# Kernel tuning notes

Hardware: AMD Instinct MI355X
Metric: run time of the kernel (lower is better)

## Reference

```python
import jax, jax.numpy as jnp
import numpy as np

N, E = 50000, 600000
IN, H, O, HEADS = 14, 128, 64, 4
EPS = 1e-5


def layer_norm(x, g, b):
    m = jnp.mean(x, axis=-1, keepdims=True)
    v = jnp.mean((x - m) ** 2, axis=-1, keepdims=True)
    return (x - m) * jax.lax.rsqrt(v + EPS) * g + b


def sage_conv(x, src, dst, W_l, b_l, W_r):
    # mean aggregation of source messages at destination, then lin_l(agg)+lin_r(x)
    s = jax.ops.segment_sum(x[src], dst, num_segments=N)            # [N,H]
    cnt = jax.ops.segment_sum(jnp.ones((src.shape[0],), x.dtype), dst, num_segments=N)
    agg = s / jnp.maximum(cnt, 1.0)[:, None]
    return agg @ W_l + b_l + x @ W_r


def gat_conv(x, src, dst, W_g, att_src, att_dst, b_g):
    # PyG GATConv with add_self_loops=True, heads=4, concat=False -> head mean
    loop = jnp.arange(N, dtype=src.dtype)
    s2 = jnp.concatenate([src, loop])
    d2 = jnp.concatenate([dst, loop])
    h = (x @ W_g).reshape(N, HEADS, O)                               # [N,4,64]
    a_s = jnp.sum(h * att_src, axis=-1)                              # [N,4]
    a_d = jnp.sum(h * att_dst, axis=-1)
    e = jax.nn.leaky_relu(a_s[s2] + a_d[d2], negative_slope=0.2)     # [E+N,4]
    m = jax.ops.segment_max(e, d2, num_segments=N)
    ex = jnp.exp(e - m[d2])
    den = jax.ops.segment_sum(ex, d2, num_segments=N)
    alpha = ex / den[d2]                                             # edge softmax
    out = jax.ops.segment_sum(h[s2] * alpha[..., None], d2, num_segments=N)
    return jnp.mean(out, axis=1) + b_g                               # [N,64]


def setup_inputs() -> dict:
    key = jax.random.key(0)
    ks = jax.random.split(key, 18)
    sc = 0.05
    return {
        'x': jax.random.normal(ks[0], (N, IN), jnp.float32),
        'edge_index': jax.random.randint(ks[1], (2, E), 0, N, dtype=jnp.int64),
        'W_in': jax.random.normal(ks[2], (IN, H), jnp.float32) * sc,
        'b_in': jnp.zeros((H,), jnp.float32),
        'W1_l': jax.random.normal(ks[3], (H, H), jnp.float32) * sc,
        'b1': jnp.zeros((H,), jnp.float32),
        'W1_r': jax.random.normal(ks[4], (H, H), jnp.float32) * sc,
        'g1': jnp.ones((H,), jnp.float32),
        'be1': jnp.zeros((H,), jnp.float32),
        'W2_l': jax.random.normal(ks[5], (H, H), jnp.float32) * sc,
        'b2': jnp.zeros((H,), jnp.float32),
        'W2_r': jax.random.normal(ks[6], (H, H), jnp.float32) * sc,
        'g2': jnp.ones((H,), jnp.float32),
        'be2': jnp.zeros((H,), jnp.float32),
        'W_g': jax.random.normal(ks[7], (H, HEADS * O), jnp.float32) * sc,
        'att_src': jax.random.normal(ks[8], (HEADS, O), jnp.float32) * sc,
        'att_dst': jax.random.normal(ks[9], (HEADS, O), jnp.float32) * sc,
        'b_g': jnp.zeros((O,), jnp.float32),
        'g3': jnp.ones((O,), jnp.float32),
        'be3': jnp.zeros((O,), jnp.float32),
    }


def reference(x, edge_index, W_in, b_in, W1_l, b1, W1_r, g1, be1,
              W2_l, b2, W2_r, g2, be2, W_g, att_src, att_dst, b_g, g3, be3):
    src, dst = edge_index[0], edge_index[1]
    h = jax.nn.relu(x @ W_in + b_in)                 # input_proj + relu (dropout: eval)
    # layer 0: SAGE + LN + relu + residual
    h_res = h
    h = jax.nn.relu(layer_norm(sage_conv(h, src, dst, W1_l, b1, W1_r), g1, be1)) + h_res
    # layer 1: SAGE + LN + relu + residual
    h_res = h
    h = jax.nn.relu(layer_norm(sage_conv(h, src, dst, W2_l, b2, W2_r), g2, be2)) + h_res
    # layer 2 (last): GAT + LN, no relu/residual (shape changes H->O anyway)
    h = layer_norm(gat_conv(h, src, dst, W_g, att_src, att_dst, b_g), g3, be3)
    return h
```

## Files before the change

### kernel.cpp

```cpp
#include <hip/hip_runtime.h>
#include <math.h>

#define EPSV 1e-5f

typedef __attribute__((ext_vector_type(8))) short short8;
typedef __attribute__((ext_vector_type(4))) float f32x4;

__device__ __forceinline__ unsigned short f2b(float f) {
  union { float f; unsigned int u; } c; c.f = f;
  unsigned int u = c.u + 0x7fffu + ((c.u >> 16) & 1u);
  return (unsigned short)(u >> 16);
}
__device__ __forceinline__ float b2f(unsigned short h) {
  union { unsigned int u; float f; } c; c.u = ((unsigned int)h) << 16;
  return c.f;
}
__device__ __forceinline__ float ub(unsigned int w, int j) {
  return (float)((w >> (8 * j)) & 0xffu);
}

__global__ void k_prep3(const float* __restrict__ Wl, const float* __restrict__ Wr,
                        const float* __restrict__ Wg, unsigned short* __restrict__ WlT,
                        unsigned short* __restrict__ WrT, unsigned short* __restrict__ WgT) {
  int id = blockIdx.x * 256 + threadIdx.x;
  if (id < 16384) {
    int n = id >> 7, k = id & 127;
    WlT[id] = f2b(Wl[k * 128 + n]);
  } else if (id < 32768) {
    int j = id - 16384; int n = j >> 7, k = j & 127;
    WrT[j] = f2b(Wr[k * 128 + n]);
  } else {
    int j = id - 32768; int n = j >> 7, k = j & 127;
    WgT[j] = f2b(Wg[k * 256 + n]);
  }
}
__global__ void k_prep2(const float* __restrict__ Wl, const float* __restrict__ Wr,
                        unsigned short* __restrict__ WlT, unsigned short* __restrict__ WrT) {
  int id = blockIdx.x * 256 + threadIdx.x;
  if (id < 16384) {
    int n = id >> 7, k = id & 127;
    WlT[id] = f2b(Wl[k * 128 + n]);
  } else {
    int j = id - 16384; int n = j >> 7, k = j & 127;
    WrT[j] = f2b(Wr[k * 128 + n]);
  }
}

__global__ void k_proj(const float* __restrict__ x, const float* __restrict__ W,
                       const float* __restrict__ b, unsigned short* __restrict__ h16,
                       unsigned char* __restrict__ h8, float2* __restrict__ hmeta, int nN) {
  int t = blockIdx.x * 256 + threadIdx.x;
  int n = t >> 6;
  if (n >= nN) return;
  int lane = t & 63;
  const float* xr = x + (size_t)n * 14;
  float acc0 = b[lane], acc1 = b[lane + 64];
#pragma unroll
  for (int k = 0; k < 14; ++k) {
    float xv = xr[k];
    acc0 = fmaf(xv, W[k * 128 + lane], acc0);
    acc1 = fmaf(xv, W[k * 128 + lane + 64], acc1);
  }
  float o0 = fmaxf(acc0, 0.f), o1 = fmaxf(acc1, 0.f);
  h16[(size_t)n * 128 + lane] = f2b(o0);
  h16[(size_t)n * 128 + lane + 64] = f2b(o1);
  float rmin = fminf(o0, o1), rmax = fmaxf(o0, o1);
#pragma unroll
  for (int m = 1; m <= 32; m <<= 1) {
    rmin = fminf(rmin, __shfl_xor(rmin, m));
    rmax = fmaxf(rmax, __shfl_xor(rmax, m));
  }
  float scale = (rmax - rmin) * (1.f / 255.f);
  float invq = (rmax > rmin) ? 255.f / (rmax - rmin) : 0.f;
  h8[(size_t)n * 128 + lane] = (unsigned char)(int)rintf((o0 - rmin) * invq);
  h8[(size_t)n * 128 + lane + 64] = (unsigned char)(int)rintf((o1 - rmin) * invq);
  if (lane == 0) hmeta[n] = make_float2(scale, rmin);
}

__global__ void k_count_int(const int* __restrict__ dst, int* __restrict__ cnt, int E_) {
  int e = blockIdx.x * 256 + threadIdx.x;
  if (e < E_) atomicAdd(&cnt[dst[e]], 1);
}

__global__ void k_scan1(const int* __restrict__ cnt, int* __restrict__ incl,
                        int* __restrict__ bsum, int nN) {
  __shared__ int sh[256];
  int tid = threadIdx.x;
  int i = blockIdx.x * 256 + tid;
  int v = (i < nN) ? cnt[i] : 0;
  sh[tid] = v;
  __syncthreads();
#pragma unroll
  for (int off = 1; off < 256; off <<= 1) {
    int t = (tid >= off) ? sh[tid - off] : 0;
    __syncthreads();
    sh[tid] += t;
    __syncthreads();
  }
  if (i < nN) incl[i] = sh[tid];
  if (tid == 255) bsum[blockIdx.x] = sh[255];
}

__global__ void k_scan2(int* __restrict__ bsum, int nb) {
  __shared__ int sh[256];
  int tid = threadIdx.x;
  int v = (tid < nb) ? bsum[tid] : 0;
  sh[tid] = v;
  __syncthreads();
#pragma unroll
  for (int off = 1; off < 256; off <<= 1) {
    int t = (tid >= off) ? sh[tid - off] : 0;
    __syncthreads();
    sh[tid] += t;
    __syncthreads();
  }
  if (tid < nb) bsum[tid] = sh[tid] - v;
}

__global__ void k_scan3(const int* __restrict__ incl, const int* __restrict__ bsum,
                        const int* __restrict__ cnt, int* __restrict__ rowptr, int nN) {
  int i = blockIdx.x * 256 + threadIdx.x;
  if (i < nN) rowptr[i] = incl[i] - cnt[i] + bsum[blockIdx.x];
}

__global__ void k_fill(const int* __restrict__ src, const int* __restrict__ dst,
                       const int* __restrict__ rowptr, int* __restrict__ cursor,
                       int* __restrict__ eSrc, int E_) {
  int e = blockIdx.x * 256 + threadIdx.x;
  if (e >= E_) return;
  int d = dst[e];
  int pos = rowptr[d] + atomicAdd(&cursor[d], 1);
  eSrc[pos] = src[e];
}

__global__ void k_sage_gather8(const unsigned char* __restrict__ h8,
                               const float2* __restrict__ hmeta,
                               const int* __restrict__ rowptr, const int* __restrict__ cnt,
                               const int* __restrict__ eSrc,
                               unsigned short* __restrict__ agg16, int nN) {
  int t = blockIdx.x * 256 + threadIdx.x;
  int n = t >> 4;
  if (n >= nN) return;
  int sub = t & 15;
  int fo = sub * 8;
  int beg = rowptr[n], c = cnt[n];
  float a0[8], a1[8], a2[8], a3[8];
#pragma unroll
  for (int j = 0; j < 8; ++j) { a0[j] = 0.f; a1[j] = 0.f; a2[j] = 0.f; a3[j] = 0.f; }
  float m0 = 0.f, m1 = 0.f, m2 = 0.f, m3 = 0.f;
  int i = 0;
  for (; i + 4 <= c; i += 4) {
    int s0 = eSrc[beg + i], s1 = eSrc[beg + i + 1];
    int s2 = eSrc[beg + i + 2], s3 = eSrc[beg + i + 3];
    float2 t0 = hmeta[s0], t1 = hmeta[s1], t2 = hmeta[s2], t3 = hmeta[s3];
    uint2 p0 = *(const uint2*)(h8 + (size_t)s0 * 128 + fo);
    uint2 p1 = *(const uint2*)(h8 + (size_t)s1 * 128 + fo);
    uint2 p2 = *(const uint2*)(h8 + (size_t)s2 * 128 + fo);
    uint2 p3 = *(const uint2*)(h8 + (size_t)s3 * 128 + fo);
#pragma unroll
    for (int j = 0; j < 4; ++j) {
      a0[j] = fmaf(t0.x, ub(p0.x, j), a0[j]);
      a1[j] = fmaf(t1.x, ub(p1.x, j), a1[j]);
      a2[j] = fmaf(t2.x, ub(p2.x, j), a2[j]);
      a3[j] = fmaf(t3.x, ub(p3.x, j), a3[j]);
      a0[j + 4] = fmaf(t0.x, ub(p0.y, j), a0[j + 4]);
      a1[j + 4] = fmaf(t1.x, ub(p1.y, j), a1[j + 4]);
      a2[j + 4] = fmaf(t2.x, ub(p2.y, j), a2[j + 4]);
      a3[j + 4] = fmaf(t3.x, ub(p3.y, j), a3[j + 4]);
    }
    m0 += t0.y; m1 += t1.y; m2 += t2.y; m3 += t3.y;
  }
  for (; i < c; ++i) {
    int s = eSrc[beg + i];
    float2 tm = hmeta[s];
    uint2 p = *(const uint2*)(h8 + (size_t)s * 128 + fo);
#pragma unroll
    for (int j = 0; j < 4; ++j) {
      a0[j] = fmaf(tm.x, ub(p.x, j), a0[j]);
      a0[j + 4] = fmaf(tm.x, ub(p.y, j), a0[j + 4]);
    }
    m0 += tm.y;
  }
  float mm = (m0 + m1) + (m2 + m3);
  float inv = 1.f / fmaxf((float)c, 1.f);
  short8 r;
#pragma unroll
  for (int j = 0; j < 8; ++j)
    r[j] = (short)f2b((((a0[j] + a1[j]) + (a2[j] + a3[j])) + mm) * inv);
  *(short8*)(agg16 + (size_t)n * 128 + fo) = r;
}

__global__ __launch_bounds__(256)
void k_sage_mfma(const unsigned short* __restrict__ agg16,
                 const unsigned short* __restrict__ hin16,
                 const unsigned short* __restrict__ WlT,
                 const unsigned short* __restrict__ WrT,
                 const float* __restrict__ bias, const float* __restrict__ gam,
                 const float* __restrict__ bet,
                 unsigned short* __restrict__ hout16,
                 unsigned char* __restrict__ hout8, float2* __restrict__ hmeta_o,
                 int quant, int nN) {
  __shared__ unsigned short lA[64][136];
  __shared__ unsigned short lB[128][136];
  int tid = threadIdx.x;
  int wave = tid >> 6, lane = tid & 63;
  int cl = lane & 15, g = lane >> 4;
  int rowBase = blockIdx.x * 64;
  f32x4 acc[8];
#pragma unroll
  for (int ct = 0; ct < 8; ++ct) acc[ct] = (f32x4){0.f, 0.f, 0.f, 0.f};

  int ar = tid >> 2, ap = (tid & 3) * 32;
  int br = tid >> 1, bp = (tid & 1) * 64;

  for (int half = 0; half < 2; ++half) {
    const unsigned short* At = half ? hin16 : agg16;
    const unsigned short* Bt = half ? WrT : WlT;
    if (half) __syncthreads();
    {
      int grow = rowBase + ar;
      if (grow < nN) {
        const unsigned short* sp = At + (size_t)grow * 128 + ap;
#pragma unroll
        for (int u = 0; u < 4; ++u)
          *(short8*)&lA[ar][ap + u * 8] = *(const short8*)(sp + u * 8);
      } else {
        short8 z = {0, 0, 0, 0, 0, 0, 0, 0};
#pragma unroll
        for (int u = 0; u < 4; ++u) *(short8*)&lA[ar][ap + u * 8] = z;
      }
      const unsigned short* bsp = Bt + (size_t)br * 128 + bp;
#pragma unroll
      for (int u = 0; u < 8; ++u)
        *(short8*)&lB[br][bp + u * 8] = *(const short8*)(bsp + u * 8);
    }
    __syncthreads();
#pragma unroll
    for (int ks = 0; ks < 4; ++ks) {
      short8 a = *(const short8*)&lA[wave * 16 + cl][ks * 32 + g * 8];
#pragma unroll
      for (int ct = 0; ct < 8; ++ct) {
        short8 b = *(const short8*)&lB[ct * 16 + cl][ks * 32 + g * 8];
        acc[ct] = __builtin_amdgcn_mfma_f32_16x16x32_bf16(a, b, acc[ct], 0, 0, 0);
      }
    }
  }
  __syncthreads();

  float bcol[8], gcol[8], ecol[8];
#pragma unroll
  for (int ct = 0; ct < 8; ++ct) {
    int c = ct * 16 + cl;
    bcol[ct] = bias[c]; gcol[ct] = gam[c]; ecol[ct] = bet[c];
  }
  float v[8][4];
  float s1[4] = {0.f, 0.f, 0.f, 0.f}, s2[4] = {0.f, 0.f, 0.f, 0.f};
#pragma unroll
  for (int ct = 0; ct < 8; ++ct)
#pragma unroll
    for (int r = 0; r < 4; ++r) {
      float t = acc[ct][r] + bcol[ct];
      v[ct][r] = t;
      s1[r] += t; s2[r] += t * t;
    }
#pragma unroll
  for (int m = 1; m <= 8; m <<= 1)
#pragma unroll
    for (int r = 0; r < 4; ++r) { s1[r] += __shfl_xor(s1[r], m); s2[r] += __shfl_xor(s2[r], m); }

#pragma unroll
  for (int r = 0; r < 4; ++r) {
    float mean = s1[r] * (1.f / 128.f);
    float var = s2[r] * (1.f / 128.f) - mean * mean;
    float rstd = rsqrtf(var + EPSV);
    int grow = rowBase + wave * 16 + g * 4 + r;
    if (grow < nN) {
      float o8v[8];
      float rmin = 1e30f, rmax = -1e30f;
#pragma unroll
      for (int ct = 0; ct < 8; ++ct) {
        int c = ct * 16 + cl;
        float o = fmaxf((v[ct][r] - mean) * rstd * gcol[ct] + ecol[ct], 0.f)
                  + b2f(hin16[(size_t)grow * 128 + c]);
        o8v[ct] = o;
        rmin = fminf(rmin, o); rmax = fmaxf(rmax, o);
        hout16[(size_t)grow * 128 + c] = f2b(o);
      }
      if (quant) {
#pragma unroll
        for (int m = 1; m <= 8; m <<= 1) {
          rmin = fminf(rmin, __shfl_xor(rmin, m));
          rmax = fmaxf(rmax, __shfl_xor(rmax, m));
        }
        float scale = (rmax - rmin) * (1.f / 255.f);
        float invq = (rmax > rmin) ? 255.f / (rmax - rmin) : 0.f;
#pragma unroll
        for (int ct = 0; ct < 8; ++ct) {
          int c = ct * 16 + cl;
          hout8[(size_t)grow * 128 + c] = (unsigned char)(int)rintf((o8v[ct] - rmin) * invq);
        }
        if (cl == 0) hmeta_o[grow] = make_float2(scale, rmin);
      }
    }
  }
}

__global__ __launch_bounds__(256)
void k_gatgemm(const unsigned short* __restrict__ h16, const unsigned short* __restrict__ WgT,
               const float* __restrict__ atts, const float* __restrict__ attd,
               unsigned char* __restrict__ G8, float2* __restrict__ Gmeta,
               float* __restrict__ as_, float* __restrict__ ad_, int nN) {
  __shared__ unsigned short lA[64][136];
  __shared__ unsigned short lB[128][136];
  int tid = threadIdx.x;
  int wave = tid >> 6, lane = tid & 63;
  int cl = lane & 15, g = lane >> 4;
  int rowBase = blockIdx.x * 64;
  int y = blockIdx.y;
  f32x4 acc[8];
#pragma unroll
  for (int ct = 0; ct < 8; ++ct) acc[ct] = (f32x4){0.f, 0.f, 0.f, 0.f};

  int ar = tid >> 2, ap = (tid & 3) * 32;
  int br = tid >> 1, bp = (tid & 1) * 64;
  {
    int grow = rowBase + ar;
    if (grow < nN) {
      const unsigned short* sp = h16 + (size_t)grow * 128 + ap;
#pragma unroll
      for (int u = 0; u < 4; ++u)
        *(short8*)&lA[ar][ap + u * 8] = *(const short8*)(sp + u * 8);
    } else {
      short8 z = {0, 0, 0, 0, 0, 0, 0, 0};
#pragma unroll
      for (int u = 0; u < 4; ++u) *(short8*)&lA[ar][ap + u * 8] = z;
    }
    const unsigned short* bsp = WgT + (size_t)(y * 128 + br) * 128 + bp;
#pragma unroll
    for (int u = 0; u < 8; ++u)
      *(short8*)&lB[br][bp + u * 8] = *(const short8*)(bsp + u * 8);
  }
  __syncthreads();
#pragma unroll
  for (int ks = 0; ks < 4; ++ks) {
    short8 a = *(const short8*)&lA[wave * 16 + cl][ks * 32 + g * 8];
#pragma unroll
    for (int ct = 0; ct < 8; ++ct) {
      short8 b = *(const short8*)&lB[ct * 16 + cl][ks * 32 + g * 8];
      acc[ct] = __builtin_amdgcn_mfma_f32_16x16x32_bf16(a, b, acc[ct], 0, 0, 0);
    }
  }

  float atr[8], adr[8];
#pragma unroll
  for (int ct = 0; ct < 8; ++ct) {
    int h = y * 2 + (ct >> 2);
    int w = (ct & 3) * 16 + cl;
    atr[ct] = atts[h * 64 + w];
    adr[ct] = attd[h * 64 + w];
  }
  float ps[2][4], pd[2][4];
#pragma unroll
  for (int hh = 0; hh < 2; ++hh)
#pragma unroll
    for (int r = 0; r < 4; ++r) { ps[hh][r] = 0.f; pd[hh][r] = 0.f; }

#pragma unroll
  for (int r = 0; r < 4; ++r) {
    int grow = rowBase + wave * 16 + g * 4 + r;
    float rmin = 1e30f, rmax = -1e30f;
#pragma unroll
    for (int ct = 0; ct < 8; ++ct) {
      rmin = fminf(rmin, acc[ct][r]); rmax = fmaxf(rmax, acc[ct][r]);
    }
#pragma unroll
    for (int m = 1; m <= 8; m <<= 1) {
      rmin = fminf(rmin, __shfl_xor(rmin, m));
      rmax = fmaxf(rmax, __shfl_xor(rmax, m));
    }
    float scale = (rmax - rmin) * (1.f / 255.f);
    float invq = (rmax > rmin) ? 255.f / (rmax - rmin) : 0.f;
    if (grow < nN) {
      unsigned char* op = G8 + (size_t)grow * 256 + y * 128 + cl;
#pragma unroll
      for (int ct = 0; ct < 8; ++ct)
        op[ct * 16] = (unsigned char)(int)rintf((acc[ct][r] - rmin) * invq);
      if (cl == 0) Gmeta[grow * 2 + y] = make_float2(scale, rmin);
    }
#pragma unroll
    for (int ct = 0; ct < 8; ++ct) {
      ps[ct >> 2][r] = fmaf(acc[ct][r], atr[ct], ps[ct >> 2][r]);
      pd[ct >> 2][r] = fmaf(acc[ct][r], adr[ct], pd[ct >> 2][r]);
    }
  }
#pragma unroll
  for (int m = 1; m <= 8; m <<= 1)
#pragma unroll
    for (int hh = 0; hh < 2; ++hh)
#pragma unroll
      for (int r = 0; r < 4; ++r) {
        ps[hh][r] += __shfl_xor(ps[hh][r], m);
        pd[hh][r] += __shfl_xor(pd[hh][r], m);
      }
  if (cl == 0) {
#pragma unroll
    for (int r = 0; r < 4; ++r) {
      int grow = rowBase + wave * 16 + g * 4 + r;
      if (grow < nN) {
#pragma unroll
        for (int hh = 0; hh < 2; ++hh) {
          as_[grow * 4 + y * 2 + hh] = ps[hh][r];
          ad_[grow * 4 + y * 2 + hh] = pd[hh][r];
        }
      }
    }
  }
}

__global__ void k_gat(const unsigned char* __restrict__ G8, const float2* __restrict__ Gmeta,
                      const int* __restrict__ rowptr, const int* __restrict__ cnt,
                      const int* __restrict__ eSrc,
                      const float* __restrict__ as_, const float* __restrict__ ad_,
                      const float* __restrict__ bg, const float* __restrict__ g3,
                      const float* __restrict__ be3, float* __restrict__ out, int nN) {
  int t = blockIdx.x * 256 + threadIdx.x;
  int n = t >> 5;
  if (n >= nN) return;
  int sub = t & 31;
  int h = sub >> 3;
  int yy = sub >> 4;
  int fo = sub * 8;
  float adn = ad_[n * 4 + h];

  float e0 = as_[n * 4 + h] + adn;
  e0 = fmaxf(e0, 0.2f * e0);
  float w = __expf(e0);
  float2 mts = Gmeta[n * 2 + yy];
  uint2 p = *(const uint2*)(G8 + (size_t)n * 256 + fo);
  float ws = w * mts.x;
  float a0[8], a1[8], a2[8], a3[8];
#pragma unroll
  for (int j = 0; j < 4; ++j) {
    a0[j] = ws * ub(p.x, j);
    a0[j + 4] = ws * ub(p.y, j);
    a1[j] = 0.f; a1[j + 4] = 0.f;
    a2[j] = 0.f; a2[j + 4] = 0.f;
    a3[j] = 0.f; a3[j + 4] = 0.f;
  }
  float m0 = w * mts.y, m1 = 0.f, m2 = 0.f, m3 = 0.f;
  float d0 = w, d1 = 0.f, d2 = 0.f, d3 = 0.f;

  int beg = rowptr[n], c = cnt[n];
  int i = 0;
  for (; i + 4 <= c; i += 4) {
    int s0 = eSrc[beg + i], s1i = eSrc[beg + i + 1];
    int s2i = eSrc[beg + i + 2], s3i = eSrc[beg + i + 3];
    float ev0 = as_[s0 * 4 + h] + adn;
    float ev1 = as_[s1i * 4 + h] + adn;
    float ev2 = as_[s2i * 4 + h] + adn;
    float ev3 = as_[s3i * 4 + h] + adn;
    ev0 = fmaxf(ev0, 0.2f * ev0); ev1 = fmaxf(ev1, 0.2f * ev1);
    ev2 = fmaxf(ev2, 0.2f * ev2); ev3 = fmaxf(ev3, 0.2f * ev3);
    float w0 = __expf(ev0), w1 = __expf(ev1), w2 = __expf(ev2), w3 = __expf(ev3);
    float2 t0 = Gmeta[s0 * 2 + yy], t1 = Gmeta[s1i * 2 + yy];
    float2 t2 = Gmeta[s2i * 2 + yy], t3 = Gmeta[s3i * 2 + yy];
    uint2 p0 = *(const uint2*)(G8 + (size_t)s0 * 256 + fo);
    uint2 p1 = *(const uint2*)(G8 + (size_t)s1i * 256 + fo);
    uint2 p2 = *(const uint2*)(G8 + (size_t)s2i * 256 + fo);
    uint2 p3 = *(const uint2*)(G8 + (size_t)s3i * 256 + fo);
    float ws0 = w0 * t0.x, ws1 = w1 * t1.x, ws2 = w2 * t2.x, ws3 = w3 * t3.x;
#pragma unroll
    for (int j = 0; j < 4; ++j) {
      a0[j] = fmaf(ws0, ub(p0.x, j), a0[j]);
      a1[j] = fmaf(ws1, ub(p1.x, j), a1[j]);
      a2[j] = fmaf(ws2, ub(p2.x, j), a2[j]);
      a3[j] = fmaf(ws3, ub(p3.x, j), a3[j]);
      a0[j + 4] = fmaf(ws0, ub(p0.y, j), a0[j + 4]);
      a1[j + 4] = fmaf(ws1, ub(p1.y, j), a1[j + 4]);
      a2[j + 4] = fmaf(ws2, ub(p2.y, j), a2[j + 4]);
      a3[j + 4] = fmaf(ws3, ub(p3.y, j), a3[j + 4]);
    }
    m0 = fmaf(w0, t0.y, m0); m1 = fmaf(w1, t1.y, m1);
    m2 = fmaf(w2, t2.y, m2); m3 = fmaf(w3, t3.y, m3);
    d0 += w0; d1 += w1; d2 += w2; d3 += w3;
  }
  for (; i < c; ++i) {
    int s = eSrc[beg + i];
    float ev = as_[s * 4 + h] + adn;
    ev = fmaxf(ev, 0.2f * ev);
    w = __expf(ev);
    float2 tm = Gmeta[s * 2 + yy];
    p = *(const uint2*)(G8 + (size_t)s * 256 + fo);
    float wsx = w * tm.x;
#pragma unroll
    for (int j = 0; j < 4; ++j) {
      a0[j] = fmaf(wsx, ub(p.x, j), a0[j]);
      a0[j + 4] = fmaf(wsx, ub(p.y, j), a0[j + 4]);
    }
    m0 = fmaf(w, tm.y, m0);
    d0 += w;
  }

  float den = (d0 + d1) + (d2 + d3);
  float mm = (m0 + m1) + (m2 + m3);
  float inv = 1.f / den;
  float a[8];
#pragma unroll
  for (int j = 0; j < 8; ++j)
    a[j] = (((a0[j] + a1[j]) + (a2[j] + a3[j])) + mm) * inv;

#pragma unroll
  for (int j = 0; j < 8; ++j) {
    a[j] += __shfl_xor(a[j], 8);
    a[j] += __shfl_xor(a[j], 16);
  }
  int fb = (sub & 7) * 8;
  float v[8];
  float s1 = 0.f, s2 = 0.f;
#pragma unroll
  for (int j = 0; j < 8; ++j) {
    v[j] = a[j] * 0.25f + bg[fb + j];
    s1 += v[j]; s2 += v[j] * v[j];
  }
#pragma unroll
  for (int m = 1; m <= 4; m <<= 1) { s1 += __shfl_xor(s1, m); s2 += __shfl_xor(s2, m); }
  float mean = s1 * (1.f / 64.f);
  float var = s2 * (1.f / 64.f) - mean * mean;
  float rstd = rsqrtf(var + EPSV);
  if (sub < 8) {
    float* o = out + (size_t)n * 64 + fb;
    float4 o1, o2;
    o1.x = (v[0] - mean) * rstd * g3[fb + 0] + be3[fb + 0];
    o1.y = (v[1] - mean) * rstd * g3[fb + 1] + be3[fb + 1];
    o1.z = (v[2] - mean) * rstd * g3[fb + 2] + be3[fb + 2];
    o1.w = (v[3] - mean) * rstd * g3[fb + 3] + be3[fb + 3];
    o2.x = (v[4] - mean) * rstd * g3[fb + 4] + be3[fb + 4];
    o2.y = (v[5] - mean) * rstd * g3[fb + 5] + be3[fb + 5];
    o2.z = (v[6] - mean) * rstd * g3[fb + 6] + be3[fb + 6];
    o2.w = (v[7] - mean) * rstd * g3[fb + 7] + be3[fb + 7];
    *(float4*)o = o1;
    *(float4*)(o + 4) = o2;
  }
}

extern "C" void kernel_launch(void* const* d_in, const int* in_sizes, int n_in,
                              void* d_out, int out_size, void* d_ws, size_t ws_size,
                              hipStream_t stream) {
  const float* x    = (const float*)d_in[0];
  const int*   edge = (const int*)d_in[1];
  const float* W_in = (const float*)d_in[2];
  const float* b_in = (const float*)d_in[3];
  const float* W1_l = (const float*)d_in[4];
  const float* b1   = (const float*)d_in[5];
  const float* W1_r = (const float*)d_in[6];
  const float* g1   = (const float*)d_in[7];
  const float* be1  = (const float*)d_in[8];
  const float* W2_l = (const float*)d_in[9];
  const float* b2   = (const float*)d_in[10];
  const float* W2_r = (const float*)d_in[11];
  const float* g2   = (const float*)d_in[12];
  const float* be2  = (const float*)d_in[13];
  const float* W_g  = (const float*)d_in[14];
  const float* atts = (const float*)d_in[15];
  const float* attd = (const float*)d_in[16];
  const float* b_g  = (const float*)d_in[17];
  const float* g3   = (const float*)d_in[18];
  const float* be3  = (const float*)d_in[19];

  const int nN = in_sizes[0] / 14;
  const int E_ = in_sizes[1] / 2;
  const int* src = edge;
  const int* dst = edge + E_;

  char* W = (char*)d_ws;
  unsigned short* hA16  = (unsigned short*)W; W += (size_t)nN * 128 * 2;
  unsigned short* hB16  = (unsigned short*)W; W += (size_t)nN * 128 * 2;
  unsigned short* agg16 = (unsigned short*)W; W += (size_t)nN * 128 * 2;
  unsigned short* WlT   = (unsigned short*)W; W += 16384 * 2;
  unsigned short* WrT   = (unsigned short*)W; W += 16384 * 2;
  unsigned short* WgT   = (unsigned short*)W; W += 32768 * 2;
  float* AS_ = (float*)W;                W += (size_t)nN * 4 * 4;
  float* AD_ = (float*)W;                W += (size_t)nN * 4 * 4;
  float2* metaA = (float2*)W;            W += (size_t)nN * 8;
  float2* metaB = (float2*)W;            W += (size_t)nN * 8;
  float2* Gmeta = (float2*)W;            W += (size_t)nN * 2 * 8;
  int* cntI   = (int*)W;                 W += (size_t)nN * 4;
  int* rowptr = (int*)W;                 W += (size_t)nN * 4;
  int* cursor = (int*)W;                 W += (size_t)nN * 4;
  int* incl   = (int*)W;                 W += (size_t)nN * 4;
  int* bsum   = (int*)W;                 W += 1024 * 4;
  int* eSrc   = (int*)W;                 W += (size_t)E_ * 4;
  unsigned char* h8A = (unsigned char*)W; W += (size_t)nN * 128;
  unsigned char* h8B = (unsigned char*)W; W += (size_t)nN * 128;
  unsigned char* G8  = (unsigned char*)W; W += (size_t)nN * 256;

  const int SB = (nN + 255) / 256;
  const int NB = (nN + 63) / 64;

  hipMemsetAsync(cntI, 0, (size_t)nN * sizeof(int), stream);
  hipMemsetAsync(cursor, 0, (size_t)nN * sizeof(int), stream);

  k_count_int<<<(E_ + 255) / 256, 256, 0, stream>>>(dst, cntI, E_);
  k_scan1<<<SB, 256, 0, stream>>>(cntI, incl, bsum, nN);
  k_scan2<<<1, 256, 0, stream>>>(bsum, SB);
  k_scan3<<<SB, 256, 0, stream>>>(incl, bsum, cntI, rowptr, nN);
  k_fill<<<(E_ + 255) / 256, 256, 0, stream>>>(src, dst, rowptr, cursor, eSrc, E_);

  k_prep3<<<256, 256, 0, stream>>>(W1_l, W1_r, W_g, WlT, WrT, WgT);
  k_proj<<<(nN * 64 + 255) / 256, 256, 0, stream>>>(x, W_in, b_in, hA16, h8A, metaA, nN);

  k_sage_gather8<<<(nN * 16 + 255) / 256, 256, 0, stream>>>(h8A, metaA, rowptr, cntI, eSrc, agg16, nN);
  k_sage_mfma<<<NB, 256, 0, stream>>>(agg16, hA16, WlT, WrT, b1, g1, be1, hB16, h8B, metaB, 1, nN);

  k_prep2<<<128, 256, 0, stream>>>(W2_l, W2_r, WlT, WrT);
  k_sage_gather8<<<(nN * 16 + 255) / 256, 256, 0, stream>>>(h8B, metaB, rowptr, cntI, eSrc, agg16, nN);
  k_sage_mfma<<<NB, 256, 0, stream>>>(agg16, hB16, WlT, WrT, b2, g2, be2, hA16, h8A, metaA, 0, nN);

  k_gatgemm<<<dim3(NB, 2), 256, 0, stream>>>(hA16, WgT, atts, attd, G8, Gmeta, AS_, AD_, nN);
  k_gat<<<(nN * 32 + 255) / 256, 256, 0, stream>>>(G8, Gmeta, rowptr, cntI, eSrc, AS_, AD_, b_g, g3, be3, (float*)d_out, nN);
}
```

Before: 265.5 us.

## Sort nodes by in-degree to balance gather and GAT warps

Adds a counting sort of nodes by descending in-degree (histogram, scan, scatter) and has the SAGE gather and GAT kernels process nodes in that order. Nodes with similar degree then share a wavefront, which cuts divergence and idle lanes in the per-edge loops. The cost is three extra small kernels plus a memset, and output writes that become scattered rather than sequential.

Measured after the change: 569.3 us. 114% more time.

```diff
diff --git a/kernel.cpp b/kernel.cpp
--- a/kernel.cpp
+++ b/kernel.cpp
@@ -133,14 +133,45 @@
   eSrc[pos] = src[e];
 }
 
+__global__ void k_hist(const int* __restrict__ cnt, int* __restrict__ hist, int nN) {
+  int n = blockIdx.x * 256 + threadIdx.x;
+  if (n >= nN) return;
+  int b = 255 - min(cnt[n], 255);
+  atomicAdd(&hist[b], 1);
+}
+__global__ void k_hscan(int* __restrict__ hist) {
+  __shared__ int sh[256];
+  int tid = threadIdx.x;
+  int v = hist[tid];
+  sh[tid] = v;
+  __syncthreads();
+#pragma unroll
+  for (int off = 1; off < 256; off <<= 1) {
+    int t = (tid >= off) ? sh[tid - off] : 0;
+    __syncthreads();
+    sh[tid] += t;
+    __syncthreads();
+  }
+  hist[tid] = sh[tid] - v;
+}
+__global__ void k_order(const int* __restrict__ cnt, const int* __restrict__ hbase,
+                        int* __restrict__ hcur, int* __restrict__ order, int nN) {
+  int n = blockIdx.x * 256 + threadIdx.x;
+  if (n >= nN) return;
+  int b = 255 - min(cnt[n], 255);
+  int pos = hbase[b] + atomicAdd(&hcur[b], 1);
+  order[pos] = n;
+}
+
 __global__ void k_sage_gather8(const unsigned char* __restrict__ h8,
                                const float2* __restrict__ hmeta,
                                const int* __restrict__ rowptr, const int* __restrict__ cnt,
-                               const int* __restrict__ eSrc,
+                               const int* __restrict__ eSrc, const int* __restrict__ order,
                                unsigned short* __restrict__ agg16, int nN) {
   int t = blockIdx.x * 256 + threadIdx.x;
-  int n = t >> 4;
-  if (n >= nN) return;
+  int ni = t >> 4;
+  if (ni >= nN) return;
+  int n = order[ni];
   int sub = t & 15;
   int fo = sub * 8;
   int beg = rowptr[n], c = cnt[n];
@@ -419,13 +450,14 @@
 
 __global__ void k_gat(const unsigned char* __restrict__ G8, const float2* __restrict__ Gmeta,
                       const int* __restrict__ rowptr, const int* __restrict__ cnt,
-                      const int* __restrict__ eSrc,
+                      const int* __restrict__ eSrc, const int* __restrict__ order,
                       const float* __restrict__ as_, const float* __restrict__ ad_,
                       const float* __restrict__ bg, const float* __restrict__ g3,
                       const float* __restrict__ be3, float* __restrict__ out, int nN) {
   int t = blockIdx.x * 256 + threadIdx.x;
-  int n = t >> 5;
-  if (n >= nN) return;
+  int ni = t >> 5;
+  if (ni >= nN) return;
+  int n = order[ni];
   int sub = t & 31;
   int h = sub >> 3;
   int yy = sub >> 4;
@@ -588,7 +620,10 @@
   int* rowptr = (int*)W;                 W += (size_t)nN * 4;
   int* cursor = (int*)W;                 W += (size_t)nN * 4;
   int* incl   = (int*)W;                 W += (size_t)nN * 4;
+  int* order  = (int*)W;                 W += (size_t)nN * 4;
   int* bsum   = (int*)W;                 W += 1024 * 4;
+  int* hist   = (int*)W;                 W += 256 * 4;
+  int* hcur   = (int*)W;                 W += 256 * 4;
   int* eSrc   = (int*)W;                 W += (size_t)E_ * 4;
   unsigned char* h8A = (unsigned char*)W; W += (size_t)nN * 128;
   unsigned char* h8B = (unsigned char*)W; W += (size_t)nN * 128;
@@ -599,6 +634,7 @@
 
   hipMemsetAsync(cntI, 0, (size_t)nN * sizeof(int), stream);
   hipMemsetAsync(cursor, 0, (size_t)nN * sizeof(int), stream);
+  hipMemsetAsync(hist, 0, 512 * sizeof(int), stream);
 
   k_count_int<<<(E_ + 255) / 256, 256, 0, stream>>>(dst, cntI, E_);
   k_scan1<<<SB, 256, 0, stream>>>(cntI, incl, bsum, nN);
@@ -606,16 +642,20 @@
   k_scan3<<<SB, 256, 0, stream>>>(incl, bsum, cntI, rowptr, nN);
   k_fill<<<(E_ + 255) / 256, 256, 0, stream>>>(src, dst, rowptr, cursor, eSrc, E_);
 
+  k_hist<<<SB, 256, 0, stream>>>(cntI, hist, nN);
+  k_hscan<<<1, 256, 0, stream>>>(hist);
+  k_order<<<SB, 256, 0, stream>>>(cntI, hist, hcur, order, nN);
+
   k_prep3<<<256, 256, 0, stream>>>(W1_l, W1_r, W_g, WlT, WrT, WgT);
   k_proj<<<(nN * 64 + 255) / 256, 256, 0, stream>>>(x, W_in, b_in, hA16, h8A, metaA, nN);
 
-  k_sage_gather8<<<(nN * 16 + 255) / 256, 256, 0, stream>>>(h8A, metaA, rowptr, cntI, eSrc, agg16, nN);
+  k_sage_gather8<<<(nN * 16 + 255) / 256, 256, 0, stream>>>(h8A, metaA, rowptr, cntI, eSrc, order, agg16, nN);
   k_sage_mfma<<<NB, 256, 0, stream>>>(agg16, hA16, WlT, WrT, b1, g1, be1, hB16, h8B, metaB, 1, nN);
 
   k_prep2<<<128, 256, 0, stream>>>(W2_l, W2_r, WlT, WrT);
-  k_sage_gather8<<<(nN * 16 + 255) / 256, 256, 0, stream>>>(h8B, metaB, rowptr, cntI, eSrc, agg16, nN);
+  k_sage_gather8<<<(nN * 16 + 255) / 256, 256, 0, stream>>>(h8B, metaB, rowptr, cntI, eSrc, order, agg16, nN);
   k_sage_mfma<<<NB, 256, 0, stream>>>(agg16, hB16, WlT, WrT, b2, g2, be2, hA16, h8A, metaA, 0, nN);
 
   k_gatgemm<<<dim3(NB, 2), 256, 0, stream>>>(hA16, WgT, atts, attd, G8, Gmeta, AS_, AD_, nN);
-  k_gat<<<(nN * 32 + 255) / 256, 256, 0, stream>>>(G8, Gmeta, rowptr, cntI, eSrc, AS_, AD_, b_g, g3, be3, (float*)d_out, nN);
-}
+  k_gat<<<(nN * 32 + 255) / 256, 256, 0, stream>>>(G8, Gmeta, rowptr, cntI, eSrc, order, AS_, AD_, b_g, g3, be3, (float*)d_out, nN);
+}
```

## Split per-node edge loops across more lanes with shuffle reductions; merge weight prep

Applied to the files above, without the earlier changes.

The SAGE gather now gives each node 64 lanes (4 edge slots x 16 feature lanes) instead of 16, and the GAT aggregation gives each node 64 lanes (2 edge slots x 32) instead of 32. Edges are strided across slots and partial sums are combined with cross-lane shuffles. The aim is more memory-level parallelism and shorter serial edge loops per thread, for a graph averaging about 12 in-edges per node. The two weight-transpose kernels are merged into one launched up front, and the layer-2 weights get their own buffers. In exchange it launches more threads, adds shuffle reductions, and leaves lanes idle on low-degree nodes.

New measurement: 260.7 us. Within noise of the previous version (-1.8%).

```diff
diff --git a/kernel.cpp b/kernel.cpp
--- a/kernel.cpp
+++ b/kernel.cpp
@@ -19,30 +19,28 @@
   return (float)((w >> (8 * j)) & 0xffu);
 }
 
-__global__ void k_prep3(const float* __restrict__ Wl, const float* __restrict__ Wr,
-                        const float* __restrict__ Wg, unsigned short* __restrict__ WlT,
-                        unsigned short* __restrict__ WrT, unsigned short* __restrict__ WgT) {
+__global__ void k_prep_all(const float* __restrict__ Wl1, const float* __restrict__ Wr1,
+                           const float* __restrict__ Wl2, const float* __restrict__ Wr2,
+                           const float* __restrict__ Wg,
+                           unsigned short* __restrict__ WlT1, unsigned short* __restrict__ WrT1,
+                           unsigned short* __restrict__ WlT2, unsigned short* __restrict__ WrT2,
+                           unsigned short* __restrict__ WgT) {
   int id = blockIdx.x * 256 + threadIdx.x;
   if (id < 16384) {
     int n = id >> 7, k = id & 127;
-    WlT[id] = f2b(Wl[k * 128 + n]);
+    WlT1[id] = f2b(Wl1[k * 128 + n]);
   } else if (id < 32768) {
     int j = id - 16384; int n = j >> 7, k = j & 127;
-    WrT[j] = f2b(Wr[k * 128 + n]);
-  } else {
+    WrT1[j] = f2b(Wr1[k * 128 + n]);
+  } else if (id < 49152) {
     int j = id - 32768; int n = j >> 7, k = j & 127;
+    WlT2[j] = f2b(Wl2[k * 128 + n]);
+  } else if (id < 65536) {
+    int j = id - 49152; int n = j >> 7, k = j & 127;
+    WrT2[j] = f2b(Wr2[k * 128 + n]);
+  } else if (id < 98304) {
+    int j = id - 65536; int n = j >> 7, k = j & 127;
     WgT[j] = f2b(Wg[k * 256 + n]);
-  }
-}
-__global__ void k_prep2(const float* __restrict__ Wl, const float* __restrict__ Wr,
-                        unsigned short* __restrict__ WlT, unsigned short* __restrict__ WrT) {
-  int id = blockIdx.x * 256 + threadIdx.x;
-  if (id < 16384) {
-    int n = id >> 7, k = id & 127;
-    WlT[id] = f2b(Wl[k * 128 + n]);
-  } else {
-    int j = id - 16384; int n = j >> 7, k = j & 127;
-    WrT[j] = f2b(Wr[k * 128 + n]);
   }
 }
 
@@ -139,38 +137,33 @@
                                const int* __restrict__ eSrc,
                                unsigned short* __restrict__ agg16, int nN) {
   int t = blockIdx.x * 256 + threadIdx.x;
-  int n = t >> 4;
+  int n = t >> 6;
   if (n >= nN) return;
-  int sub = t & 15;
-  int fo = sub * 8;
+  int lane = t & 63;
+  int flane = lane & 15;
+  int slot = lane >> 4;
+  int fo = flane * 8;
   int beg = rowptr[n], c = cnt[n];
-  float a0[8], a1[8], a2[8], a3[8];
-#pragma unroll
-  for (int j = 0; j < 8; ++j) { a0[j] = 0.f; a1[j] = 0.f; a2[j] = 0.f; a3[j] = 0.f; }
-  float m0 = 0.f, m1 = 0.f, m2 = 0.f, m3 = 0.f;
-  int i = 0;
-  for (; i + 4 <= c; i += 4) {
-    int s0 = eSrc[beg + i], s1 = eSrc[beg + i + 1];
-    int s2 = eSrc[beg + i + 2], s3 = eSrc[beg + i + 3];
-    float2 t0 = hmeta[s0], t1 = hmeta[s1], t2 = hmeta[s2], t3 = hmeta[s3];
+  float a0[8], a1[8];
+#pragma unroll
+  for (int j = 0; j < 8; ++j) { a0[j] = 0.f; a1[j] = 0.f; }
+  float m0 = 0.f, m1 = 0.f;
+  int i = slot;
+  for (; i + 4 < c; i += 8) {
+    int s0 = eSrc[beg + i], s1 = eSrc[beg + i + 4];
+    float2 t0 = hmeta[s0], t1 = hmeta[s1];
     uint2 p0 = *(const uint2*)(h8 + (size_t)s0 * 128 + fo);
     uint2 p1 = *(const uint2*)(h8 + (size_t)s1 * 128 + fo);
-    uint2 p2 = *(const uint2*)(h8 + (size_t)s2 * 128 + fo);
-    uint2 p3 = *(const uint2*)(h8 + (size_t)s3 * 128 + fo);
 #pragma unroll
     for (int j = 0; j < 4; ++j) {
       a0[j] = fmaf(t0.x, ub(p0.x, j), a0[j]);
       a1[j] = fmaf(t1.x, ub(p1.x, j), a1[j]);
-      a2[j] = fmaf(t2.x, ub(p2.x, j), a2[j]);
-      a3[j] = fmaf(t3.x, ub(p3.x, j), a3[j]);
       a0[j + 4] = fmaf(t0.x, ub(p0.y, j), a0[j + 4]);
       a1[j + 4] = fmaf(t1.x, ub(p1.y, j), a1[j + 4]);
-      a2[j + 4] = fmaf(t2.x, ub(p2.y, j), a2[j + 4]);
-      a3[j + 4] = fmaf(t3.x, ub(p3.y, j), a3[j + 4]);
-    }
-    m0 += t0.y; m1 += t1.y; m2 += t2.y; m3 += t3.y;
-  }
-  for (; i < c; ++i) {
+    }
+    m0 += t0.y; m1 += t1.y;
+  }
+  for (; i < c; i += 4) {
     int s = eSrc[beg + i];
     float2 tm = hmeta[s];
     uint2 p = *(const uint2*)(h8 + (size_t)s * 128 + fo);
@@ -181,13 +174,24 @@
     }
     m0 += tm.y;
   }
-  float mm = (m0 + m1) + (m2 + m3);
-  float inv = 1.f / fmaxf((float)c, 1.f);
-  short8 r;
-#pragma unroll
-  for (int j = 0; j < 8; ++j)
-    r[j] = (short)f2b((((a0[j] + a1[j]) + (a2[j] + a3[j])) + mm) * inv);
-  *(short8*)(agg16 + (size_t)n * 128 + fo) = r;
+  float a[8];
+  float mm = m0 + m1;
+#pragma unroll
+  for (int j = 0; j < 8; ++j) a[j] = a0[j] + a1[j];
+#pragma unroll
+  for (int j = 0; j < 8; ++j) {
+    a[j] += __shfl_xor(a[j], 16);
+    a[j] += __shfl_xor(a[j], 32);
+  }
+  mm += __shfl_xor(mm, 16);
+  mm += __shfl_xor(mm, 32);
+  if (slot == 0) {
+    float inv = 1.f / fmaxf((float)c, 1.f);
+    short8 r;
+#pragma unroll
+    for (int j = 0; j < 8; ++j) r[j] = (short)f2b((a[j] + mm) * inv);
+    *(short8*)(agg16 + (size_t)n * 128 + fo) = r;
+  }
 }
 
 __global__ __launch_bounds__(256)
@@ -424,73 +428,66 @@
                       const float* __restrict__ bg, const float* __restrict__ g3,
                       const float* __restrict__ be3, float* __restrict__ out, int nN) {
   int t = blockIdx.x * 256 + threadIdx.x;
-  int n = t >> 5;
+  int n = t >> 6;
   if (n >= nN) return;
-  int sub = t & 31;
+  int lane = t & 63;
+  int sub = lane & 31;
+  int slot = lane >> 5;
   int h = sub >> 3;
   int yy = sub >> 4;
   int fo = sub * 8;
   float adn = ad_[n * 4 + h];
 
-  float e0 = as_[n * 4 + h] + adn;
-  e0 = fmaxf(e0, 0.2f * e0);
-  float w = __expf(e0);
-  float2 mts = Gmeta[n * 2 + yy];
-  uint2 p = *(const uint2*)(G8 + (size_t)n * 256 + fo);
-  float ws = w * mts.x;
-  float a0[8], a1[8], a2[8], a3[8];
-#pragma unroll
-  for (int j = 0; j < 4; ++j) {
-    a0[j] = ws * ub(p.x, j);
-    a0[j + 4] = ws * ub(p.y, j);
-    a1[j] = 0.f; a1[j + 4] = 0.f;
-    a2[j] = 0.f; a2[j + 4] = 0.f;
-    a3[j] = 0.f; a3[j + 4] = 0.f;
-  }
-  float m0 = w * mts.y, m1 = 0.f, m2 = 0.f, m3 = 0.f;
-  float d0 = w, d1 = 0.f, d2 = 0.f, d3 = 0.f;
+  float a0[8], a1[8];
+#pragma unroll
+  for (int j = 0; j < 8; ++j) { a0[j] = 0.f; a1[j] = 0.f; }
+  float m0 = 0.f, m1 = 0.f, d0 = 0.f, d1 = 0.f;
+
+  if (slot == 0) {
+    float e0 = as_[n * 4 + h] + adn;
+    e0 = fmaxf(e0, 0.2f * e0);
+    float w = __expf(e0);
+    float2 mts = Gmeta[n * 2 + yy];
+    uint2 p = *(const uint2*)(G8 + (size_t)n * 256 + fo);
+    float ws = w * mts.x;
+#pragma unroll
+    for (int j = 0; j < 4; ++j) {
+      a0[j] = ws * ub(p.x, j);
+      a0[j + 4] = ws * ub(p.y, j);
+    }
+    m0 = w * mts.y;
+    d0 = w;
+  }
 
   int beg = rowptr[n], c = cnt[n];
-  int i = 0;
-  for (; i + 4 <= c; i += 4) {
-    int s0 = eSrc[beg + i], s1i = eSrc[beg + i + 1];
-    int s2i = eSrc[beg + i + 2], s3i = eSrc[beg + i + 3];
+  int i = slot;
+  for (; i + 2 < c; i += 4) {
+    int s0 = eSrc[beg + i], s1i = eSrc[beg + i + 2];
     float ev0 = as_[s0 * 4 + h] + adn;
     float ev1 = as_[s1i * 4 + h] + adn;
-    float ev2 = as_[s2i * 4 + h] + adn;
-    float ev3 = as_[s3i * 4 + h] + adn;
     ev0 = fmaxf(ev0, 0.2f * ev0); ev1 = fmaxf(ev1, 0.2f * ev1);
-    ev2 = fmaxf(ev2, 0.2f * ev2); ev3 = fmaxf(ev3, 0.2f * ev3);
-    float w0 = __expf(ev0), w1 = __expf(ev1), w2 = __expf(ev2), w3 = __expf(ev3);
+    float w0 = __expf(ev0), w1 = __expf(ev1);
     float2 t0 = Gmeta[s0 * 2 + yy], t1 = Gmeta[s1i * 2 + yy];
-    float2 t2 = Gmeta[s2i * 2 + yy], t3 = Gmeta[s3i * 2 + yy];
     uint2 p0 = *(const uint2*)(G8 + (size_t)s0 * 256 + fo);
     uint2 p1 = *(const uint2*)(G8 + (size_t)s1i * 256 + fo);
-    uint2 p2 = *(const uint2*)(G8 + (size_t)s2i * 256 + fo);
-    uint2 p3 = *(const uint2*)(G8 + (size_t)s3i * 256 + fo);
-    float ws0 = w0 * t0.x, ws1 = w1 * t1.x, ws2 = w2 * t2.x, ws3 = w3 * t3.x;
+    float ws0 = w0 * t0.x, ws1 = w1 * t1.x;
 #pragma unroll
     for (int j = 0; j < 4; ++j) {
       a0[j] = fmaf(ws0, ub(p0.x, j), a0[j]);
       a1[j] = fmaf(ws1, ub(p1.x, j), a1[j]);
-      a2[j] = fmaf(ws2, ub(p2.x, j), a2[j]);
-      a3[j] = fmaf(ws3, ub(p3.x, j), a3[j]);
       a0[j + 4] = fmaf(ws0, ub(p0.y, j), a0[j + 4]);
       a1[j + 4] = fmaf(ws1, ub(p1.y, j), a1[j + 4]);
-      a2[j + 4] = fmaf(ws2, ub(p2.y, j), a2[j + 4]);
-      a3[j + 4] = fmaf(ws3, ub(p3.y, j), a3[j + 4]);
     }
     m0 = fmaf(w0, t0.y, m0); m1 = fmaf(w1, t1.y, m1);
-    m2 = fmaf(w2, t2.y, m2); m3 = fmaf(w3, t3.y, m3);
-    d0 += w0; d1 += w1; d2 += w2; d3 += w3;
-  }
-  for (; i < c; ++i) {
+    d0 += w0; d1 += w1;
+  }
+  for (; i < c; i += 2) {
     int s = eSrc[beg + i];
     float ev = as_[s * 4 + h] + adn;
     ev = fmaxf(ev, 0.2f * ev);
-    w = __expf(ev);
+    float w = __expf(ev);
     float2 tm = Gmeta[s * 2 + yy];
-    p = *(const uint2*)(G8 + (size_t)s * 256 + fo);
+    uint2 p = *(const uint2*)(G8 + (size_t)s * 256 + fo);
     float wsx = w * tm.x;
 #pragma unroll
     for (int j = 0; j < 4; ++j) {
@@ -501,13 +498,19 @@
     d0 += w;
   }
 
-  float den = (d0 + d1) + (d2 + d3);
-  float mm = (m0 + m1) + (m2 + m3);
+  float den = d0 + d1;
+  float mm = m0 + m1;
+  float a[8];
+#pragma unroll
+  for (int j = 0; j < 8; ++j) a[j] = a0[j] + a1[j];
+#pragma unroll
+  for (int j = 0; j < 8; ++j) a[j] += __shfl_xor(a[j], 32);
+  den += __shfl_xor(den, 32);
+  mm += __shfl_xor(mm, 32);
+
   float inv = 1.f / den;
-  float a[8];
-#pragma unroll
-  for (int j = 0; j < 8; ++j)
-    a[j] = (((a0[j] + a1[j]) + (a2[j] + a3[j])) + mm) * inv;
+#pragma unroll
+  for (int j = 0; j < 8; ++j) a[j] = (a[j] + mm) * inv;
 
 #pragma unroll
   for (int j = 0; j < 8; ++j) {
@@ -527,7 +530,7 @@
   float mean = s1 * (1.f / 64.f);
   float var = s2 * (1.f / 64.f) - mean * mean;
   float rstd = rsqrtf(var + EPSV);
-  if (sub < 8) {
+  if (lane < 8) {
     float* o = out + (size_t)n * 64 + fb;
     float4 o1, o2;
     o1.x = (v[0] - mean) * rstd * g3[fb + 0] + be3[fb + 0];
@@ -576,8 +579,10 @@
   unsigned short* hA16  = (unsigned short*)W; W += (size_t)nN * 128 * 2;
   unsigned short* hB16  = (unsigned short*)W; W += (size_t)nN * 128 * 2;
   unsigned short* agg16 = (unsigned short*)W; W += (size_t)nN * 128 * 2;
-  unsigned short* WlT   = (unsigned short*)W; W += 16384 * 2;
-  unsigned short* WrT   = (unsigned short*)W; W += 16384 * 2;
+  unsigned short* WlT1  = (unsigned short*)W; W += 16384 * 2;
+  unsigned short* WrT1  = (unsigned short*)W; W += 16384 * 2;
+  unsigned short* WlT2  = (unsigned short*)W; W += 16384 * 2;
+  unsigned short* WrT2  = (unsigned short*)W; W += 16384 * 2;
   unsigned short* WgT   = (unsigned short*)W; W += 32768 * 2;
   float* AS_ = (float*)W;                W += (size_t)nN * 4 * 4;
   float* AD_ = (float*)W;                W += (size_t)nN * 4 * 4;
@@ -600,22 +605,22 @@
   hipMemsetAsync(cntI, 0, (size_t)nN * sizeof(int), stream);
   hipMemsetAsync(cursor, 0, (size_t)nN * sizeof(int), stream);
 
+  k_prep_all<<<384, 256, 0, stream>>>(W1_l, W1_r, W2_l, W2_r, W_g, WlT1, WrT1, WlT2, WrT2, WgT);
+
   k_count_int<<<(E_ + 255) / 256, 256, 0, stream>>>(dst, cntI, E_);
   k_scan1<<<SB, 256, 0, stream>>>(cntI, incl, bsum, nN);
   k_scan2<<<1, 256, 0, stream>>>(bsum, SB);
   k_scan3<<<SB, 256, 0, stream>>>(incl, bsum, cntI, rowptr, nN);
   k_fill<<<(E_ + 255) / 256, 256, 0, stream>>>(src, dst, rowptr, cursor, eSrc, E_);
 
-  k_prep3<<<256, 256, 0, stream>>>(W1_l, W1_r, W_g, WlT, WrT, WgT);
   k_proj<<<(nN * 64 + 255) / 256, 256, 0, stream>>>(x, W_in, b_in, hA16, h8A, metaA, nN);
 
-  k_sage_gather8<<<(nN * 16 + 255) / 256, 256, 0, stream>>>(h8A, metaA, rowptr, cntI, eSrc, agg16, nN);
-  k_sage_mfma<<<NB, 256, 0, stream>>>(agg16, hA16, WlT, WrT, b1, g1, be1, hB16, h8B, metaB, 1, nN);
-
-  k_prep2<<<128, 256, 0, stream>>>(W2_l, W2_r, WlT, WrT);
-  k_sage_gather8<<<(nN * 16 + 255) / 256, 256, 0, stream>>>(h8B, metaB, rowptr, cntI, eSrc, agg16, nN);
-  k_sage_mfma<<<NB, 256, 0, stream>>>(agg16, hB16, WlT, WrT, b2, g2, be2, hA16, h8A, metaA, 0, nN);
+  k_sage_gather8<<<(nN * 64 + 255) / 256, 256, 0, stream>>>(h8A, metaA, rowptr, cntI, eSrc, agg16, nN);
+  k_sage_mfma<<<NB, 256, 0, stream>>>(agg16, hA16, WlT1, WrT1, b1, g1, be1, hB16, h8B, metaB, 1, nN);
+
+  k_sage_gather8<<<(nN * 64 + 255) / 256, 256, 0, stream>>>(h8B, metaB, rowptr, cntI, eSrc, agg16, nN);
+  k_sage_mfma<<<NB, 256, 0, stream>>>(agg16, hB16, WlT2, WrT2, b2, g2, be2, hA16, h8A, metaA, 0, nN);
 
   k_gatgemm<<<dim3(NB, 2), 256, 0, stream>>>(hA16, WgT, atts, attd, G8, Gmeta, AS_, AD_, nN);
-  k_gat<<<(nN * 32 + 255) / 256, 256, 0, stream>>>(G8, Gmeta, rowptr, cntI, eSrc, AS_, AD_, b_g, g3, be3, (float*)d_out, nN);
-}
+  k_gat<<<(nN * 64 + 255) / 256, 256, 0, stream>>>(G8, Gmeta, rowptr, cntI, eSrc, AS_, AD_, b_g, g3, be3, (float*)d_out, nN);
+}
```
